# Performance work log

Hardware: AMD Instinct MI355X
Metric: run time of the kernel (lower is better)

The kernel has to match this reference:

```python
import jax, jax.numpy as jnp
import numpy as np
import math

B, S, D = 2, 1024, 2048
NH, NKV, HD = 16, 8, 128
NREP = NH // NKV
WINDOW = 256  # = max_seq_len; ReRoPE window


def _rope(x, cos, sin):
    # x: (b, s, h, d); cos/sin broadcastable to (b, s, h, d//2). Interleaved pairs (llama2.c style).
    b, s, h, d = x.shape
    xr, xi = x[..., ::2], x[..., 1::2]
    or_ = xr * cos - xi * sin
    oi = xr * sin + xi * cos
    return jnp.stack([or_, oi], axis=-1).reshape(b, s, h, d)


def setup_inputs() -> dict:
    key = jax.random.key(0)
    kx, kq, kk, kv, ko = jax.random.split(key, 5)
    # real RoPE tables (theta=10000), per-position, half head dim
    inv = 1.0 / (10000.0 ** (np.arange(0, HD, 2, dtype=np.float32) / HD))
    fr = np.outer(np.arange(S, dtype=np.float32), inv).astype(np.float32)  # (S, HD//2)
    sc = 0.02
    return {
        "x": jax.random.normal(kx, (B, S, D), jnp.float32),
        "freqs_cos": jnp.asarray(np.cos(fr)),
        "freqs_sin": jnp.asarray(np.sin(fr)),
        "wq": jax.random.normal(kq, (D, NH * HD), jnp.float32) * sc,
        "wk": jax.random.normal(kk, (D, NKV * HD), jnp.float32) * sc,
        "wv": jax.random.normal(kv, (D, NKV * HD), jnp.float32) * sc,
        "wo": jax.random.normal(ko, (NH * HD, D), jnp.float32) * sc,
    }


def reference(x, freqs_cos, freqs_sin, wq, wk, wv, wo):
    b, s, _ = x.shape
    xq = (x @ wq).reshape(b, s, NH, HD)
    xk = (x @ wk).reshape(b, s, NKV, HD)
    xv = (x @ wv).reshape(b, s, NKV, HD)

    cos = freqs_cos[:s][None, :, None, :]
    sin = freqs_sin[:s][None, :, None, :]
    q1 = _rope(xq, cos, sin)   # standard RoPE
    k1 = _rope(xk, cos, sin)

    # ReRoPE: queries rotated at the fixed clamp position = window; keys unrotated
    cw = freqs_cos[WINDOW][None, None, None, :]
    sw = freqs_sin[WINDOW][None, None, None, :]
    q2 = _rope(xq, cw, sw)
    k2 = xk

    rep = lambda a: jnp.repeat(a, NREP, axis=2)          # repeat_kv (GQA)
    heads = lambda a: a.transpose(0, 2, 1, 3)            # (b, h, s, d)
    q1, k1, v = heads(q1), heads(rep(k1)), heads(rep(xv))
    q2, k2 = heads(q2), heads(rep(k2))

    scale = 1.0 / math.sqrt(HD)
    s1 = jnp.einsum("bhqd,bhkd->bhqk", q1, k1) * scale
    s2 = jnp.einsum("bhqd,bhkd->bhqk", q2, k2) * scale

    i = jnp.arange(s)[:, None]
    j = jnp.arange(s)[None, :]
    causal = j <= i
    rect = causal & (j > i - WINDOW)                     # rectified_mask band
    scores = jnp.where(rect, s1, s2)
    scores = jnp.where(causal, scores, -jnp.inf)         # mask_inf (causal)

    attn = jax.nn.softmax(scores.astype(jnp.float32), axis=-1).astype(x.dtype)
    out = jnp.einsum("bhqk,bhkd->bhqd", attn, v)
    out = out.transpose(0, 2, 1, 3).reshape(b, s, NH * HD)
    return out @ wo
```

## Files before the change

kernel.cpp:

```cpp
#include <hip/hip_runtime.h>
#include <hip/hip_bf16.h>

#define BDIM 2
#define SDIM 1024
#define DDIM 2048
#define NH 16
#define NKV 8
#define HD 128
#define WINDOW 256

typedef __bf16 bf16;
typedef __bf16 bf16x4 __attribute__((ext_vector_type(4)));
typedef __bf16 bf16x8 __attribute__((ext_vector_type(8)));
typedef float f32x4 __attribute__((ext_vector_type(4)));

#define L2E 1.44269504088896341f

__device__ inline bf16x8 load8(const bf16* p) { return *reinterpret_cast<const bf16x8*>(p); }

__device__ __forceinline__ void gl_lds16(const bf16* g, bf16* l) {
  __builtin_amdgcn_global_load_lds(
      (__attribute__((address_space(1))) void*)g,
      (__attribute__((address_space(3))) void*)l,
      16, 0, 0);
}

__global__ __launch_bounds__(256) void cast_f32_bf16(const float* __restrict__ src,
                                                     bf16* __restrict__ dst) {
  long i = ((long)blockIdx.x * 256 + threadIdx.x) * 8;
  float4 a = *(const float4*)(src + i);
  float4 b = *(const float4*)(src + i + 4);
  bf16x8 o;
  o[0] = (bf16)a.x; o[1] = (bf16)a.y; o[2] = (bf16)a.z; o[3] = (bf16)a.w;
  o[4] = (bf16)b.x; o[5] = (bf16)b.y; o[6] = (bf16)b.z; o[7] = (bf16)b.w;
  *(bf16x8*)(dst + i) = o;
}

__global__ __launch_bounds__(256) void wtrans_all(const float* __restrict__ wq,
                                                  const float* __restrict__ wk,
                                                  const float* __restrict__ wv,
                                                  const float* __restrict__ wo,
                                                  bf16* __restrict__ wqkvT,
                                                  bf16* __restrict__ woT) {
  __shared__ bf16 tile[32][33];
  int z = blockIdx.z;
  const float* src; bf16* dst; int C;
  if (z == 0)      { src = wq; dst = wqkvT;                 C = 2048; }
  else if (z == 1) { src = wk; dst = wqkvT + 2048L * 2048;  C = 1024; }
  else if (z == 2) { src = wv; dst = wqkvT + 3072L * 2048;  C = 1024; }
  else             { src = wo; dst = woT;                   C = 2048; }
  int c0 = blockIdx.x * 32, r0 = blockIdx.y * 32;
  if (c0 >= C) return;
  int x = threadIdx.x, y = threadIdx.y;
  for (int yy = y; yy < 32; yy += 8)
    tile[yy][x] = (bf16)src[(long)(r0 + yy) * C + c0 + x];
  __syncthreads();
  for (int yy = y; yy < 32; yy += 8)
    dst[(long)(c0 + yy) * 2048 + r0 + x] = tile[x][yy];
}

__global__ __launch_bounds__(256) void vtrans(const bf16* __restrict__ qkv,
                                              bf16* __restrict__ vT) {
  __shared__ bf16 tile[32][33];
  int s0 = blockIdx.x * 32, d0 = blockIdx.y * 32;
  int z = blockIdx.z;
  int b = z >> 3, kv = z & 7;
  const bf16* src = qkv + ((long)b * SDIM) * 4096 + 3072 + kv * 128;
  bf16* dst = vT + (long)z * 128 * 1024;
  int x = threadIdx.x, y = threadIdx.y;
  for (int yy = y; yy < 32; yy += 8)
    tile[yy][x] = src[(long)(s0 + yy) * 4096 + d0 + x];
  __syncthreads();
  for (int yy = y; yy < 32; yy += 8)
    dst[(long)(d0 + yy) * 1024 + s0 + x] = tile[x][yy];
}

#define BK 64
template <typename OT>
__global__ __launch_bounds__(256) void gemm_bt_lds(const bf16* __restrict__ A,
                                                   const bf16* __restrict__ Bt,
                                                   OT* __restrict__ C,
                                                   int M, int N, int K) {
  __shared__ bf16 As[128 * BK];
  __shared__ bf16 Bs[128 * BK];
  int m0 = blockIdx.y * 128, n0 = blockIdx.x * 128;
  int t = threadIdx.x;
  int wid = t >> 6, lane = t & 63;
  int wm = (wid >> 1) * 64, wn = (wid & 1) * 64;
  int fm = lane & 15, quad = lane >> 4;
  f32x4 acc[4][4] = {};
  for (int k0 = 0; k0 < K; k0 += BK) {
    for (int p = 0; p < 4; ++p) {
      int idx = p * 256 + t;
      int row = idx >> 3, ccs = idx & 7;
      int gcol = ((ccs ^ (row & 7)) * 8);
      gl_lds16(&A[(long)(m0 + row) * K + k0 + gcol], &As[idx * 8]);
      gl_lds16(&Bt[(long)(n0 + row) * K + k0 + gcol], &Bs[idx * 8]);
    }
    __syncthreads();
    for (int ks = 0; ks < BK; ks += 32) {
      int cc = (ks >> 3) + quad;
      bf16x8 af[4], bfr[4];
      for (int i = 0; i < 4; ++i) {
        int fr = wm + i * 16 + fm;
        af[i] = load8(&As[(fr * 8 + (cc ^ (fr & 7))) * 8]);
      }
      for (int i = 0; i < 4; ++i) {
        int fr = wn + i * 16 + fm;
        bfr[i] = load8(&Bs[(fr * 8 + (cc ^ (fr & 7))) * 8]);
      }
      for (int i = 0; i < 4; ++i)
        for (int j = 0; j < 4; ++j)
          acc[i][j] = __builtin_amdgcn_mfma_f32_16x16x32_bf16(af[i], bfr[j], acc[i][j], 0, 0, 0);
    }
    __syncthreads();
  }
  for (int i = 0; i < 4; ++i)
    for (int j = 0; j < 4; ++j)
      for (int r = 0; r < 4; ++r) {
        int row = m0 + wm + i * 16 + quad * 4 + r;
        int col = n0 + wn + j * 16 + fm;
        C[(long)row * N + col] = (OT)acc[i][j][r];
      }
}

__global__ __launch_bounds__(256) void rope_qk(const bf16* __restrict__ qkv,
                                               const float* __restrict__ fc,
                                               const float* __restrict__ fs,
                                               bf16* __restrict__ q1,
                                               bf16* __restrict__ q2,
                                               bf16* __restrict__ k1) {
  int idx = blockIdx.x * 256 + threadIdx.x;
  if (idx < 2 * 1024 * 1024) {
    int row = idx >> 10;
    int rem = idx & 1023;
    int h = rem >> 6, d = rem & 63;
    int s = row & (SDIM - 1);
    long src = (long)row * 4096 + h * 128 + 2 * d;
    float xr = (float)qkv[src], xi = (float)qkv[src + 1];
    const float scale = 0.08838834764831845f;
    float c = fc[s * 64 + d], sn = fs[s * 64 + d];
    long dst = (long)row * 2048 + h * 128 + 2 * d;
    q1[dst]     = (bf16)((xr * c - xi * sn) * scale);
    q1[dst + 1] = (bf16)((xr * sn + xi * c) * scale);
    float cw = fc[WINDOW * 64 + d], sw = fs[WINDOW * 64 + d];
    q2[dst]     = (bf16)((xr * cw - xi * sw) * scale);
    q2[dst + 1] = (bf16)((xr * sw + xi * cw) * scale);
  } else {
    int i2 = idx - 2 * 1024 * 1024;
    int row = i2 >> 9;
    int rem = i2 & 511;
    int kv = rem >> 6, d = rem & 63;
    int s = row & (SDIM - 1);
    long src = (long)row * 4096 + 2048 + kv * 128 + 2 * d;
    float xr = (float)qkv[src], xi = (float)qkv[src + 1];
    float c = fc[s * 64 + d], sn = fs[s * 64 + d];
    long dst = (long)row * 1024 + kv * 128 + 2 * d;
    k1[dst]     = (bf16)(xr * c - xi * sn);
    k1[dst + 1] = (bf16)(xr * sn + xi * c);
  }
}

__global__ __launch_bounds__(256) void attn_kernel(const bf16* __restrict__ q1,
                                                   const bf16* __restrict__ q2,
                                                   const bf16* __restrict__ k1,
                                                   const bf16* __restrict__ qkv,
                                                   const bf16* __restrict__ vT,
                                                   bf16* __restrict__ aout) {
  __shared__ bf16 Ks[16384];
  __shared__ bf16 VTs[8192];
  __shared__ bf16 Pl[4][16][72];
  __shared__ float stats[4][16];

  int h = blockIdx.y;
  int b = blockIdx.z;
  int tile = b ? (15 - blockIdx.x) : blockIdx.x;
  int kv = h >> 1;
  int t = threadIdx.x;
  int w = t >> 6, lane = t & 63;
  int m = lane & 15, quad = lane >> 4;

  const bf16* k1g0 = k1 + ((long)b * SDIM) * 1024 + kv * 128;
  const bf16* k2g0 = qkv + ((long)b * SDIM) * 4096 + 2048 + kv * 128;
  const bf16* vtg0 = vT + ((long)(b * NKV + kv)) * 128 * 1024;

  int t0 = tile * 64;
  int i0w = t0 + w * 16;

  const bf16* q1p = q1 + ((long)(b * SDIM + i0w + m)) * 2048 + h * 128 + quad * 8;
  const bf16* q2p = q2 + ((long)(b * SDIM + i0w + m)) * 2048 + h * 128 + quad * 8;
  bf16x8 q1f[4], q2f[4];
  for (int kc = 0; kc < 4; ++kc) {
    q1f[kc] = load8(q1p + kc * 32);
    q2f[kc] = load8(q2p + kc * 32);
  }

  f32x4 o[8] = {};
  float mrow = -INFINITY, lrow = 0.f;

  for (int j0 = 0; j0 < t0 + 64; j0 += 64) {
    bool c1 = (j0 + 63 > t0 - WINDOW);
    bool c2 = (j0 <= t0 + 63 - WINDOW);
    __syncthreads();
    for (int p = 0; p < 4; ++p) {
      int idx = p * 256 + t;
      int kr = idx >> 4, kcs = idx & 15;
      int kg = (kcs ^ (kr & 15)) * 8;
      if (c1) gl_lds16(&k1g0[(long)(j0 + kr) * 1024 + kg], &Ks[idx * 8]);
      if (c2) gl_lds16(&k2g0[(long)(j0 + kr) * 4096 + kg], &Ks[8192 + idx * 8]);
      int vd = idx >> 3, vcs = idx & 7;
      int vg = (vcs ^ (vd & 7)) * 8;
      gl_lds16(&vtg0[(long)vd * 1024 + j0 + vg], &VTs[idx * 8]);
    }
    __syncthreads();

    if (j0 < i0w + 16) {
      bool need1 = (j0 + 63 > i0w - WINDOW);
      bool need2 = (j0 <= i0w + 15 - WINDOW);
      f32x4 s1[4] = {}, s2[4] = {};
      if (need1)
        for (int st = 0; st < 4; ++st)
          for (int kc = 0; kc < 4; ++kc) {
            int cc = kc * 4 + quad;
            s1[st] = __builtin_amdgcn_mfma_f32_16x16x32_bf16(
                load8(&Ks[((st * 16 + m) * 16 + (cc ^ m)) * 8]), q1f[kc], s1[st], 0, 0, 0);
          }
      if (need2)
        for (int st = 0; st < 4; ++st)
          for (int kc = 0; kc < 4; ++kc) {
            int cc = kc * 4 + quad;
            s2[st] = __builtin_amdgcn_mfma_f32_16x16x32_bf16(
                load8(&Ks[8192 + ((st * 16 + m) * 16 + (cc ^ m)) * 8]), q2f[kc], s2[st], 0, 0, 0);
          }
      int i = i0w + m;
      float sv[4][4];
      for (int st = 0; st < 4; ++st)
        for (int r = 0; r < 4; ++r) {
          int j = j0 + st * 16 + quad * 4 + r;
          float v;
          if (j > i) v = -INFINITY;
          else if (j > i - WINDOW) v = s1[st][r];
          else v = s2[st][r];
          sv[st][r] = v;
        }
      float bm = -INFINITY;
      for (int st = 0; st < 4; ++st)
        for (int r = 0; r < 4; ++r) bm = fmaxf(bm, sv[st][r]);
      bm = fmaxf(bm, __shfl_xor(bm, 16, 64));
      bm = fmaxf(bm, __shfl_xor(bm, 32, 64));
      float mnew = fmaxf(mrow, bm);
      float alpha = exp2f((mrow - mnew) * L2E);
      float rs = 0.f;
      for (int st = 0; st < 4; ++st) {
        bf16x4 pk;
        for (int r = 0; r < 4; ++r) {
          float pvv = exp2f((sv[st][r] - mnew) * L2E);
          rs += pvv;
          pk[r] = (bf16)pvv;
        }
        *(bf16x4*)&Pl[w][m][st * 16 + quad * 4] = pk;
      }
      rs += __shfl_xor(rs, 16, 64);
      rs += __shfl_xor(rs, 32, 64);
      lrow = lrow * alpha + rs;
      mrow = mnew;
      if (lane < 16) stats[w][lane] = alpha;
      f32x4 av = *(f32x4*)&stats[w][quad * 4];
      for (int n8 = 0; n8 < 8; ++n8)
        for (int r = 0; r < 4; ++r) o[n8][r] *= av[r];
      for (int kc = 0; kc < 2; ++kc) {
        bf16x8 af = load8(&Pl[w][m][kc * 32 + quad * 8]);
        int cc = kc * 4 + quad;
        for (int n8 = 0; n8 < 8; ++n8) {
          int d = n8 * 16 + m;
          o[n8] = __builtin_amdgcn_mfma_f32_16x16x32_bf16(
              af, load8(&VTs[(d * 8 + (cc ^ (d & 7))) * 8]), o[n8], 0, 0, 0);
        }
      }
    }
  }

  if (lane < 16) stats[w][lane] = lrow;
  __builtin_amdgcn_s_waitcnt(0);
  f32x4 lv = *(f32x4*)&stats[w][quad * 4];
  for (int n8 = 0; n8 < 8; ++n8)
    for (int r = 0; r < 4; ++r) {
      int row = i0w + quad * 4 + r;
      float val = o[n8][r] / lv[r];
      aout[((long)(b * SDIM + row)) * 2048 + h * 128 + n8 * 16 + m] = (bf16)val;
    }
}

extern "C" void kernel_launch(void* const* d_in, const int* in_sizes, int n_in,
                              void* d_out, int out_size, void* d_ws, size_t ws_size,
                              hipStream_t stream) {
  const float* x  = (const float*)d_in[0];
  const float* fc = (const float*)d_in[1];
  const float* fs = (const float*)d_in[2];
  const float* wq = (const float*)d_in[3];
  const float* wk = (const float*)d_in[4];
  const float* wv = (const float*)d_in[5];
  const float* wo = (const float*)d_in[6];
  float* out = (float*)d_out;

  bf16* wqkvT = (bf16*)d_ws;
  bf16* woT   = wqkvT + 4096L * 2048;
  bf16* xb    = woT + 2048L * 2048;
  bf16* qkv   = xb + 2048L * 2048;
  bf16* q1    = qkv + 2048L * 4096;
  bf16* q2    = q1 + 2048L * 2048;
  bf16* k1b   = q2 + 2048L * 2048;
  bf16* vT    = k1b + 2048L * 1024;
  bf16* aout  = vT + 2048L * 1024;

  cast_f32_bf16<<<2048, 256, 0, stream>>>(x, xb);
  wtrans_all<<<dim3(64, 64, 4), dim3(32, 8), 0, stream>>>(wq, wk, wv, wo, wqkvT, woT);

  gemm_bt_lds<bf16><<<dim3(32, 16), 256, 0, stream>>>(xb, wqkvT, qkv, 2048, 4096, 2048);

  rope_qk<<<12288, 256, 0, stream>>>(qkv, fc, fs, q1, q2, k1b);
  vtrans<<<dim3(32, 4, 16), dim3(32, 8), 0, stream>>>(qkv, vT);

  attn_kernel<<<dim3(16, 16, 2), 256, 0, stream>>>(q1, q2, k1b, qkv, vT, aout);

  gemm_bt_lds<float><<<dim3(16, 16), 256, 0, stream>>>(aout, woT, out, 2048, 2048, 2048);
}
```

Before: 260.0 us.

## Fuse RoPE into QKV GEMM epilogue and write split q/k/v buffers

The QKV projection GEMM now applies standard and ReRoPE rotations in its epilogue. It uses a lane shuffle to fetch the paired element and writes q1, q2, k1, k2 and v directly, which removes the separate rope_qk kernel and its full read of the qkv intermediate. The attention and V-transpose kernels now read compact 1024-stride k2 and v buffers. The cost is a heavier epilogue with scattered 2-byte stores and per-element table loads inside the GEMM.

```diff
diff --git a/kernel.cpp b/kernel.cpp
--- a/kernel.cpp
+++ b/kernel.cpp
@@ -59,17 +59,17 @@
     dst[(long)(c0 + yy) * 2048 + r0 + x] = tile[x][yy];
 }
 
-__global__ __launch_bounds__(256) void vtrans(const bf16* __restrict__ qkv,
+__global__ __launch_bounds__(256) void vtrans(const bf16* __restrict__ vc,
                                               bf16* __restrict__ vT) {
   __shared__ bf16 tile[32][33];
   int s0 = blockIdx.x * 32, d0 = blockIdx.y * 32;
   int z = blockIdx.z;
   int b = z >> 3, kv = z & 7;
-  const bf16* src = qkv + ((long)b * SDIM) * 4096 + 3072 + kv * 128;
+  const bf16* src = vc + ((long)b * SDIM) * 1024 + kv * 128;
   bf16* dst = vT + (long)z * 128 * 1024;
   int x = threadIdx.x, y = threadIdx.y;
   for (int yy = y; yy < 32; yy += 8)
-    tile[yy][x] = src[(long)(s0 + yy) * 4096 + d0 + x];
+    tile[yy][x] = src[(long)(s0 + yy) * 1024 + d0 + x];
   __syncthreads();
   for (int yy = y; yy < 32; yy += 8)
     dst[(long)(d0 + yy) * 1024 + s0 + x] = tile[x][yy];
@@ -124,47 +124,108 @@
       }
 }
 
-__global__ __launch_bounds__(256) void rope_qk(const bf16* __restrict__ qkv,
-                                               const float* __restrict__ fc,
-                                               const float* __restrict__ fs,
-                                               bf16* __restrict__ q1,
-                                               bf16* __restrict__ q2,
-                                               bf16* __restrict__ k1) {
-  int idx = blockIdx.x * 256 + threadIdx.x;
-  if (idx < 2 * 1024 * 1024) {
-    int row = idx >> 10;
-    int rem = idx & 1023;
-    int h = rem >> 6, d = rem & 63;
-    int s = row & (SDIM - 1);
-    long src = (long)row * 4096 + h * 128 + 2 * d;
-    float xr = (float)qkv[src], xi = (float)qkv[src + 1];
+__global__ __launch_bounds__(256) void gemm_qkv(const bf16* __restrict__ A,
+                                                const bf16* __restrict__ Bt,
+                                                const float* __restrict__ fc,
+                                                const float* __restrict__ fs,
+                                                bf16* __restrict__ q1,
+                                                bf16* __restrict__ q2,
+                                                bf16* __restrict__ k1,
+                                                bf16* __restrict__ k2,
+                                                bf16* __restrict__ vc) {
+  const int K = 2048, N = 4096;
+  __shared__ bf16 As[128 * BK];
+  __shared__ bf16 Bs[128 * BK];
+  int m0 = blockIdx.y * 128, n0 = blockIdx.x * 128;
+  int t = threadIdx.x;
+  int wid = t >> 6, lane = t & 63;
+  int wm = (wid >> 1) * 64, wn = (wid & 1) * 64;
+  int fm = lane & 15, quad = lane >> 4;
+  f32x4 acc[4][4] = {};
+  for (int k0 = 0; k0 < K; k0 += BK) {
+    for (int p = 0; p < 4; ++p) {
+      int idx = p * 256 + t;
+      int row = idx >> 3, ccs = idx & 7;
+      int gcol = ((ccs ^ (row & 7)) * 8);
+      gl_lds16(&A[(long)(m0 + row) * K + k0 + gcol], &As[idx * 8]);
+      gl_lds16(&Bt[(long)(n0 + row) * K + k0 + gcol], &Bs[idx * 8]);
+    }
+    __syncthreads();
+    for (int ks = 0; ks < BK; ks += 32) {
+      int cc = (ks >> 3) + quad;
+      bf16x8 af[4], bfr[4];
+      for (int i = 0; i < 4; ++i) {
+        int fr = wm + i * 16 + fm;
+        af[i] = load8(&As[(fr * 8 + (cc ^ (fr & 7))) * 8]);
+      }
+      for (int i = 0; i < 4; ++i) {
+        int fr = wn + i * 16 + fm;
+        bfr[i] = load8(&Bs[(fr * 8 + (cc ^ (fr & 7))) * 8]);
+      }
+      for (int i = 0; i < 4; ++i)
+        for (int j = 0; j < 4; ++j)
+          acc[i][j] = __builtin_amdgcn_mfma_f32_16x16x32_bf16(af[i], bfr[j], acc[i][j], 0, 0, 0);
+    }
+    __syncthreads();
+  }
+
+  int n0h = n0 >> 7;
+  float sgn = (lane & 1) ? 1.f : -1.f;
+  if (n0h < 16) {
     const float scale = 0.08838834764831845f;
-    float c = fc[s * 64 + d], sn = fs[s * 64 + d];
-    long dst = (long)row * 2048 + h * 128 + 2 * d;
-    q1[dst]     = (bf16)((xr * c - xi * sn) * scale);
-    q1[dst + 1] = (bf16)((xr * sn + xi * c) * scale);
-    float cw = fc[WINDOW * 64 + d], sw = fs[WINDOW * 64 + d];
-    q2[dst]     = (bf16)((xr * cw - xi * sw) * scale);
-    q2[dst + 1] = (bf16)((xr * sw + xi * cw) * scale);
+    for (int j = 0; j < 4; ++j) {
+      int col = wn + j * 16 + fm;
+      int dp = col >> 1;
+      float cw = fc[WINDOW * 64 + dp];
+      float sw = fs[WINDOW * 64 + dp] * sgn;
+      for (int i = 0; i < 4; ++i)
+        for (int r = 0; r < 4; ++r) {
+          int row = m0 + wm + i * 16 + quad * 4 + r;
+          int s = row & (SDIM - 1);
+          float v = acc[i][j][r];
+          float pp = __shfl_xor(v, 1, 64);
+          float c = fc[s * 64 + dp];
+          float sn = fs[s * 64 + dp] * sgn;
+          long dst = (long)row * 2048 + n0h * 128 + col;
+          q1[dst] = (bf16)((v * c + pp * sn) * scale);
+          q2[dst] = (bf16)((v * cw + pp * sw) * scale);
+        }
+    }
+  } else if (n0h < 24) {
+    int kvh = n0h - 16;
+    for (int j = 0; j < 4; ++j) {
+      int col = wn + j * 16 + fm;
+      int dp = col >> 1;
+      for (int i = 0; i < 4; ++i)
+        for (int r = 0; r < 4; ++r) {
+          int row = m0 + wm + i * 16 + quad * 4 + r;
+          int s = row & (SDIM - 1);
+          float v = acc[i][j][r];
+          float pp = __shfl_xor(v, 1, 64);
+          float c = fc[s * 64 + dp];
+          float sn = fs[s * 64 + dp] * sgn;
+          long dst = (long)row * 1024 + kvh * 128 + col;
+          k1[dst] = (bf16)(v * c + pp * sn);
+          k2[dst] = (bf16)v;
+        }
+    }
   } else {
-    int i2 = idx - 2 * 1024 * 1024;
-    int row = i2 >> 9;
-    int rem = i2 & 511;
-    int kv = rem >> 6, d = rem & 63;
-    int s = row & (SDIM - 1);
-    long src = (long)row * 4096 + 2048 + kv * 128 + 2 * d;
-    float xr = (float)qkv[src], xi = (float)qkv[src + 1];
-    float c = fc[s * 64 + d], sn = fs[s * 64 + d];
-    long dst = (long)row * 1024 + kv * 128 + 2 * d;
-    k1[dst]     = (bf16)(xr * c - xi * sn);
-    k1[dst + 1] = (bf16)(xr * sn + xi * c);
+    int vv = n0h - 24;
+    for (int j = 0; j < 4; ++j) {
+      int col = wn + j * 16 + fm;
+      for (int i = 0; i < 4; ++i)
+        for (int r = 0; r < 4; ++r) {
+          int row = m0 + wm + i * 16 + quad * 4 + r;
+          vc[(long)row * 1024 + vv * 128 + col] = (bf16)acc[i][j][r];
+        }
+    }
   }
 }
 
 __global__ __launch_bounds__(256) void attn_kernel(const bf16* __restrict__ q1,
                                                    const bf16* __restrict__ q2,
                                                    const bf16* __restrict__ k1,
-                                                   const bf16* __restrict__ qkv,
+                                                   const bf16* __restrict__ k2,
                                                    const bf16* __restrict__ vT,
                                                    bf16* __restrict__ aout) {
   __shared__ bf16 Ks[16384];
@@ -181,7 +242,7 @@
   int m = lane & 15, quad = lane >> 4;
 
   const bf16* k1g0 = k1 + ((long)b * SDIM) * 1024 + kv * 128;
-  const bf16* k2g0 = qkv + ((long)b * SDIM) * 4096 + 2048 + kv * 128;
+  const bf16* k2g0 = k2 + ((long)b * SDIM) * 1024 + kv * 128;
   const bf16* vtg0 = vT + ((long)(b * NKV + kv)) * 128 * 1024;
 
   int t0 = tile * 64;
@@ -207,7 +268,7 @@
       int kr = idx >> 4, kcs = idx & 15;
       int kg = (kcs ^ (kr & 15)) * 8;
       if (c1) gl_lds16(&k1g0[(long)(j0 + kr) * 1024 + kg], &Ks[idx * 8]);
-      if (c2) gl_lds16(&k2g0[(long)(j0 + kr) * 4096 + kg], &Ks[8192 + idx * 8]);
+      if (c2) gl_lds16(&k2g0[(long)(j0 + kr) * 1024 + kg], &Ks[8192 + idx * 8]);
       int vd = idx >> 3, vcs = idx & 7;
       int vg = (vcs ^ (vd & 7)) * 8;
       gl_lds16(&vtg0[(long)vd * 1024 + j0 + vg], &VTs[idx * 8]);
@@ -306,22 +367,22 @@
   bf16* wqkvT = (bf16*)d_ws;
   bf16* woT   = wqkvT + 4096L * 2048;
   bf16* xb    = woT + 2048L * 2048;
-  bf16* qkv   = xb + 2048L * 2048;
-  bf16* q1    = qkv + 2048L * 4096;
+  bf16* q1    = xb + 2048L * 2048;
   bf16* q2    = q1 + 2048L * 2048;
   bf16* k1b   = q2 + 2048L * 2048;
-  bf16* vT    = k1b + 2048L * 1024;
+  bf16* k2b   = k1b + 2048L * 1024;
+  bf16* vcb   = k2b + 2048L * 1024;
+  bf16* vT    = vcb + 2048L * 1024;
   bf16* aout  = vT + 2048L * 1024;
 
   cast_f32_bf16<<<2048, 256, 0, stream>>>(x, xb);
   wtrans_all<<<dim3(64, 64, 4), dim3(32, 8), 0, stream>>>(wq, wk, wv, wo, wqkvT, woT);
 
-  gemm_bt_lds<bf16><<<dim3(32, 16), 256, 0, stream>>>(xb, wqkvT, qkv, 2048, 4096, 2048);
-
-  rope_qk<<<12288, 256, 0, stream>>>(qkv, fc, fs, q1, q2, k1b);
-  vtrans<<<dim3(32, 4, 16), dim3(32, 8), 0, stream>>>(qkv, vT);
-
-  attn_kernel<<<dim3(16, 16, 2), 256, 0, stream>>>(q1, q2, k1b, qkv, vT, aout);
+  gemm_qkv<<<dim3(32, 16), 256, 0, stream>>>(xb, wqkvT, fc, fs, q1, q2, k1b, k2b, vcb);
+
+  vtrans<<<dim3(32, 4, 16), dim3(32, 8), 0, stream>>>(vcb, vT);
+
+  attn_kernel<<<dim3(16, 16, 2), 256, 0, stream>>>(q1, q2, k1b, k2b, vT, aout);
 
   gemm_bt_lds<float><<<dim3(16, 16), 256, 0, stream>>>(aout, woT, out, 2048, 2048, 2048);
 }
```

New measurement: 258.2 us. About the same (-0.7%).
